# Kernel tuning notes

Hardware: AMD Instinct MI355X
Metric: run time of the kernel (lower is better)

## Reference

```python
import jax, jax.numpy as jnp
import numpy as np

B, K, NV, H, T = 4, 2, 32, 16, 4096
G = K * NV                 # conv groups = 64
OPG = 2 * (NV + H)         # out channels per group = 96 (instantaneous doubles channels)
TEMPERATURE = 1.0


def setup_inputs() -> dict:
    key = jax.random.key(0)
    k1, k2, k3 = jax.random.split(key, 3)
    x = jax.random.normal(k1, (B, G * H, T), dtype=jnp.float32)
    W = jax.random.normal(k2, (G, OPG, H), dtype=jnp.float32) * (1.0 / np.sqrt(H))
    b = jax.random.normal(k3, (G, OPG), dtype=jnp.float32) * 0.01
    return {"x": x, "W": W, "b": b}


def reference(x, W, b):
    # pad one zero step at end of sequence (ConstantPad1d((0,1),0))
    xp = jnp.pad(x, ((0, 0), (0, 0), (0, 1)))            # (B, G*H, T+1)
    xg = xp.reshape(B, G, H, T + 1)
    # TCN modeled as grouped pointwise conv: per-group linear over channel dim
    y = jnp.einsum('bgdt,god->bgot', xg, W) + b[None, :, :, None]  # (B, G, OPG, T+1)
    # split temporal / instantaneous branches with the causal shift
    y = y.reshape(B * K, NV, 2, NV + H, T + 1)
    xt = y[:, :, 0, :, :-1]                               # (B*K, NV, NV+H, T)
    xi = y[:, :, 1, :, 1:]                                # (B*K, NV, NV+H, T)
    # split attention logits (first NV channels) and context (last H channels)
    ctx = jnp.concatenate([xt[:, :, NV:, :], xi[:, :, NV:, :]], axis=1)   # (B*K, 2*NV, H, T)
    att = jnp.concatenate([xt[:, :, :NV, :], xi[:, :, :NV, :]], axis=2)   # (B*K, NV, 2*NV, T)
    att = jax.nn.softmax(att / TEMPERATURE, axis=2)
    out = jnp.einsum('bijt,bjdt->bidt', att, ctx)         # (B*K, NV, H, T)
    out = out.reshape(B, K * NV * H, T)
    attn = att.reshape(B, K, NV, 2 * NV, T)
    return out, attn
```

## Files before the change

kernel.cpp:

```cpp
#include <hip/hip_runtime.h>
#include <stdint.h>

#define T_    4096
#define XGS   74
#define AIS32 33
#define ATS32 1056
#define CTS16 1056
#define RSW   33

typedef _Float16 h2 __attribute__((ext_vector_type(2)));

static __device__ __forceinline__ float dot2(uint32_t a, uint32_t b, float c) {
#if __has_builtin(__builtin_amdgcn_fdot2)
    return __builtin_amdgcn_fdot2(__builtin_bit_cast(h2, a), __builtin_bit_cast(h2, b), c, false);
#else
    h2 ha = __builtin_bit_cast(h2, a), hb = __builtin_bit_cast(h2, b);
    return fmaf((float)ha.x, (float)hb.x, fmaf((float)ha.y, (float)hb.y, c));
#endif
}
static __device__ __forceinline__ float exp2a(float x) {
#if __has_builtin(__builtin_amdgcn_exp2f)
    return __builtin_amdgcn_exp2f(x);
#else
    return exp2f(x);
#endif
}
static __device__ __forceinline__ uint16_t f2h(float f) {
    _Float16 h = (_Float16)f; return __builtin_bit_cast(uint16_t, h);
}
static __device__ __forceinline__ float h2f(uint16_t u) {
    return (float)__builtin_bit_cast(_Float16, u);
}
static __device__ __forceinline__ uint32_t pk2(float lo, float hi) {
    return __builtin_bit_cast(uint32_t, __builtin_amdgcn_cvt_pkrtz(lo, hi));
}
static __device__ __forceinline__ int stg_ix(int rp, int t) {
    return rp * 9 + 2 * (rp >> 4) + t;
}

__global__ __launch_bounds__(512, 2)
void tamcad_kernel(const float* __restrict__ x, const float* __restrict__ W,
                   const float* __restrict__ bias, float* __restrict__ out)
{
    __shared__ uint32_t As32[8448];
    __shared__ uint32_t Cs32[4224];
    __shared__ uint32_t xs32[2368];
    __shared__ uint32_t stg [2336];
    __shared__ float    rs  [264];
    uint16_t* Cs16 = (uint16_t*)Cs32;

    const int tid   = threadIdx.x;
    const int bk    = blockIdx.x >> 6;
    const int chunk = blockIdx.x & 63;
    const int b     = bk >> 1;
    const int k     = bk & 1;

    const int oq   = tid & 15;
    const int g    = tid >> 4;
    const int slot = oq >> 3;

    uint32_t wp2[6][8]; float breg[6]; bool isl[6];
    int cofs[6]; int aofs[3]; bool acat[3];
    #pragma unroll
    for (int r = 0; r < 6; ++r) {
        const int o = oq * 6 + r;
        const float4* wp = reinterpret_cast<const float4*>(W + (((size_t)(k*32+g))*96 + o)*16);
        float4 w0 = wp[0], w1 = wp[1], w2 = wp[2], w3 = wp[3];
        wp2[r][0] = pk2(w0.x, w0.y); wp2[r][1] = pk2(w0.z, w0.w);
        wp2[r][2] = pk2(w1.x, w1.y); wp2[r][3] = pk2(w1.z, w1.w);
        wp2[r][4] = pk2(w2.x, w2.y); wp2[r][5] = pk2(w2.z, w2.w);
        wp2[r][6] = pk2(w3.x, w3.y); wp2[r][7] = pk2(w3.z, w3.w);
        breg[r] = bias[(k*32+g)*96 + o];
        cofs[r] = 0;
        if (o < 32)       isl[r] = true;
        else if (o < 48) { isl[r] = false; cofs[r] = (o-32)*66 + g; }
        else if (o < 80)  isl[r] = true;
        else             { isl[r] = false; cofs[r] = (o-80)*66 + 32 + g; }
    }
    #pragma unroll
    for (int p = 0; p < 3; ++p) {
        const int oe = oq*6 + 2*p;
        if (oe < 32)                   { acat[p] = true;  aofs[p] = g*AIS32 + (oe >> 1); }
        else if (oe >= 48 && oe < 80)  { acat[p] = true;  aofs[p] = g*AIS32 + ((oe-16) >> 1); }
        else                           { acat[p] = false; aofs[p] = 0; }
    }

    const float* xrow = x + ((size_t)b*1024 + (size_t)(k*32+g)*16 + oq) * (size_t)T_;

    float4 pA, pB; float pS;
    {
        const float* gp = xrow + chunk*64;
        pA = *(const float4*)gp; pB = *(const float4*)(gp + 4); pS = gp[8];
    }

    for (int l = 0; l <= 8; ++l) {
        const int t0p = chunk*64 + (l-1)*8;

        if (l > 0) {
            if (tid >= 256) {
                const int q = tid - 256, j = q & 63, jb = j >> 1, jh = j & 1;
                float* attn_base = out + (size_t)4*1024*(size_t)T_;
                #pragma unroll
                for (int rr = 0; rr < 8; ++rr) {
                    const int i = (q >> 6) + 4*rr;
                    float av[8];
                    #pragma unroll
                    for (int u = 0; u < 8; ++u) {
                        uint32_t w = As32[u*ATS32 + i*AIS32 + jb];
                        av[u] = h2f(jh ? (uint16_t)(w >> 16) : (uint16_t)(w & 0xFFFF))
                              * rs[u*RSW + i];
                    }
                    float* tp2 = attn_base + (((size_t)bk*32 + i)*64 + j)*(size_t)T_ + t0p;
                    *(float4*)(tp2+0) = make_float4(av[0],av[1],av[2],av[3]);
                    *(float4*)(tp2+4) = make_float4(av[4],av[5],av[6],av[7]);
                }
            } else {
                const int t  = tid >> 5;
                const int r5 = tid & 31;
                const int i0 = (r5 >> 2) * 4;
                const int d0 = (r5 & 3) * 4;
                const int ab = t*ATS32 + i0*AIS32;
                const int cb = t*528 + d0*33;
                float acc[4][4];
                #pragma unroll
                for (int ii = 0; ii < 4; ++ii)
                    #pragma unroll
                    for (int dd = 0; dd < 4; ++dd) acc[ii][dd] = 0.f;
                #pragma unroll 4
                for (int jp = 0; jp < 32; ++jp) {
                    uint32_t a0 = As32[ab+jp],    a1 = As32[ab+33+jp];
                    uint32_t a2 = As32[ab+66+jp], a3 = As32[ab+99+jp];
                    uint32_t c0 = Cs32[cb+jp],    c1 = Cs32[cb+33+jp];
                    uint32_t c2 = Cs32[cb+66+jp], c3 = Cs32[cb+99+jp];
                    acc[0][0]=dot2(a0,c0,acc[0][0]); acc[0][1]=dot2(a0,c1,acc[0][1]);
                    acc[0][2]=dot2(a0,c2,acc[0][2]); acc[0][3]=dot2(a0,c3,acc[0][3]);
                    acc[1][0]=dot2(a1,c0,acc[1][0]); acc[1][1]=dot2(a1,c1,acc[1][1]);
                    acc[1][2]=dot2(a1,c2,acc[1][2]); acc[1][3]=dot2(a1,c3,acc[1][3]);
                    acc[2][0]=dot2(a2,c0,acc[2][0]); acc[2][1]=dot2(a2,c1,acc[2][1]);
                    acc[2][2]=dot2(a2,c2,acc[2][2]); acc[2][3]=dot2(a2,c3,acc[2][3]);
                    acc[3][0]=dot2(a3,c0,acc[3][0]); acc[3][1]=dot2(a3,c1,acc[3][1]);
                    acc[3][2]=dot2(a3,c2,acc[3][2]); acc[3][3]=dot2(a3,c3,acc[3][3]);
                }
                #pragma unroll
                for (int ii = 0; ii < 4; ++ii) {
                    const float rv = rs[t*RSW + i0 + ii];
                    const int rp = (i0+ii)*8 + (d0 >> 1);
                    stg[stg_ix(rp,   t)] = pk2(acc[ii][0]*rv, acc[ii][1]*rv);
                    stg[stg_ix(rp+1, t)] = pk2(acc[ii][2]*rv, acc[ii][3]*rv);
                }
            }
        }
        if (l < 8) {
            float vals[9] = { pA.x,pA.y,pA.z,pA.w, pB.x,pB.y,pB.z,pB.w, pS };
            #pragma unroll
            for (int i = 0; i < 9; ++i) {
                float mine  = vals[i];
                float other = __shfl_xor(mine, 1);
                if (((i ^ oq) & 1) == 0) {
                    uint32_t pk = (oq & 1) ? pk2(other, mine) : pk2(mine, other);
                    xs32[g*XGS + i*8 + (oq >> 1)] = pk;
                }
            }
            if (l < 7) {
                const int t0n = chunk*64 + (l+1)*8;
                const float* gp = xrow + t0n;
                pA = *(const float4*)gp; pB = *(const float4*)(gp + 4);
                pS = ((t0n + 8) < T_) ? gp[8] : 0.0f;
            }
        }
        __syncthreads();

        if (l > 0) {
            const int rp = tid >> 1, hi = tid & 1, base = stg_ix(rp, 0);
            float ov[8];
            #pragma unroll
            for (int u = 0; u < 8; ++u) {
                uint32_t w = stg[base + u];
                ov[u] = h2f(hi ? (uint16_t)(w >> 16) : (uint16_t)(w & 0xFFFF));
            }
            float* op = out + ((size_t)b*1024 + k*512 + tid)*(size_t)T_ + t0p;
            *(float4*)(op+0) = make_float4(ov[0],ov[1],ov[2],ov[3]);
            *(float4*)(op+4) = make_float4(ov[4],ov[5],ov[6],ov[7]);
        }
        if (l < 8) {
            float asum[8];
            #pragma unroll
            for (int q = 0; q < 8; ++q) {
                const uint32_t* xp = xs32 + g*XGS + (q + slot)*8;
                uint4 xa = *(const uint4*)xp;
                uint4 xb = *(const uint4*)(xp + 4);
                uint32_t xw[8] = { xa.x,xa.y,xa.z,xa.w, xb.x,xb.y,xb.z,xb.w };
                float v[6]; float s = 0.f;
                #pragma unroll
                for (int r = 0; r < 6; ++r) {
                    float y = breg[r];
                    #pragma unroll
                    for (int dd = 0; dd < 8; ++dd) y = dot2(wp2[r][dd], xw[dd], y);
                    const float e = exp2a(fmaf(y, 1.44269504089f, -4.0f));
                    v[r] = isl[r] ? e : y;
                    s   += isl[r] ? e : 0.f;
                }
                #pragma unroll
                for (int p = 0; p < 3; ++p) {
                    if (acat[p]) {
                        As32[q*ATS32 + aofs[p]] = pk2(v[2*p], v[2*p+1]);
                    } else {
                        Cs16[q*CTS16 + cofs[2*p]]   = f2h(v[2*p]);
                        Cs16[q*CTS16 + cofs[2*p+1]] = f2h(v[2*p+1]);
                    }
                }
                asum[q] = s;
            }
            #pragma unroll
            for (int sft = 1; sft < 16; sft <<= 1) {
                #pragma unroll
                for (int q = 0; q < 8; ++q) asum[q] += __shfl_xor(asum[q], sft);
            }
            if (oq == 0) {
                #pragma unroll
                for (int q = 0; q < 8; ++q)
                    rs[q*RSW + g] = __builtin_amdgcn_rcpf(asum[q]);
            }
        }
        if (l < 8) __syncthreads();
    }
}

extern "C" void kernel_launch(void* const* d_in, const int* in_sizes, int n_in,
                              void* d_out, int out_size, void* d_ws, size_t ws_size,
                              hipStream_t stream) {
    const float* x  = (const float*)d_in[0];
    const float* W  = (const float*)d_in[1];
    const float* bs = (const float*)d_in[2];
    float* out = (float*)d_out;
    tamcad_kernel<<<dim3(512), dim3(512), 0, stream>>>(x, W, bs, out);
}
```

Baseline: 285.6 us.

## Double block size to 1024 threads and split per-thread work in half

Moves the block from 512 to 1024 threads. Each thread now computes 3 output channels instead of 6, loads half an x row segment, and handles a 2x4 instead of a 4x4 attention-context tile. The A and C shared buffers are merged into one fp16 array, so every channel does a single scalar fp16 store. The aim is more waves per block to hide latency and fewer registers per thread. The cost is more shuffle-reduction steps, less register reuse per thread, and tighter occupancy limits at 1024 threads.

```diff
diff --git a/kernel.cpp b/kernel.cpp
--- a/kernel.cpp
+++ b/kernel.cpp
@@ -3,9 +3,10 @@
 
 #define T_    4096
 #define XGS   74
-#define AIS32 33
-#define ATS32 1056
+#define ATS16 2112
+#define AIS16 66
 #define CTS16 1056
+#define CSB16 16896
 #define RSW   33
 
 typedef _Float16 h2 __attribute__((ext_vector_type(2)));
@@ -38,16 +39,16 @@
     return rp * 9 + 2 * (rp >> 4) + t;
 }
 
-__global__ __launch_bounds__(512, 2)
+__global__ __launch_bounds__(1024, 4)
 void tamcad_kernel(const float* __restrict__ x, const float* __restrict__ W,
                    const float* __restrict__ bias, float* __restrict__ out)
 {
-    __shared__ uint32_t As32[8448];
-    __shared__ uint32_t Cs32[4224];
+    __shared__ uint16_t ACs16[CSB16 + 8 * CTS16];
     __shared__ uint32_t xs32[2368];
     __shared__ uint32_t stg [2336];
     __shared__ float    rs  [264];
-    uint16_t* Cs16 = (uint16_t*)Cs32;
+    const uint32_t* As32r = (const uint32_t*)ACs16;
+    const uint32_t* Cs32r = (const uint32_t*)(ACs16 + CSB16);
 
     const int tid   = threadIdx.x;
     const int bk    = blockIdx.x >> 6;
@@ -55,15 +56,17 @@
     const int b     = bk >> 1;
     const int k     = bk & 1;
 
-    const int oq   = tid & 15;
-    const int g    = tid >> 4;
-    const int slot = oq >> 3;
-
-    uint32_t wp2[6][8]; float breg[6]; bool isl[6];
-    int cofs[6]; int aofs[3]; bool acat[3];
+    const int g  = tid >> 5;
+    const int m  = tid & 31;
+    const int d  = m >> 1;
+    const int h  = m & 1;
+    const int oq = m;
+    const int slot = m >> 4;
+
+    uint32_t wp2[3][8]; float breg[3]; int sofs[3]; bool isl[3];
     #pragma unroll
-    for (int r = 0; r < 6; ++r) {
-        const int o = oq * 6 + r;
+    for (int r = 0; r < 3; ++r) {
+        const int o = oq * 3 + r;
         const float4* wp = reinterpret_cast<const float4*>(W + (((size_t)(k*32+g))*96 + o)*16);
         float4 w0 = wp[0], w1 = wp[1], w2 = wp[2], w3 = wp[3];
         wp2[r][0] = pk2(w0.x, w0.y); wp2[r][1] = pk2(w0.z, w0.w);
@@ -71,42 +74,64 @@
         wp2[r][4] = pk2(w2.x, w2.y); wp2[r][5] = pk2(w2.z, w2.w);
         wp2[r][6] = pk2(w3.x, w3.y); wp2[r][7] = pk2(w3.z, w3.w);
         breg[r] = bias[(k*32+g)*96 + o];
-        cofs[r] = 0;
-        if (o < 32)       isl[r] = true;
-        else if (o < 48) { isl[r] = false; cofs[r] = (o-32)*66 + g; }
-        else if (o < 80)  isl[r] = true;
-        else             { isl[r] = false; cofs[r] = (o-80)*66 + 32 + g; }
+        if (o < 32)      { isl[r] = true;  sofs[r] = g*AIS16 + o; }
+        else if (o < 48) { isl[r] = false; sofs[r] = CSB16 + (o-32)*AIS16 + g; }
+        else if (o < 80) { isl[r] = true;  sofs[r] = g*AIS16 + (o-16); }
+        else             { isl[r] = false; sofs[r] = CSB16 + (o-80)*AIS16 + 32 + g; }
     }
-    #pragma unroll
-    for (int p = 0; p < 3; ++p) {
-        const int oe = oq*6 + 2*p;
-        if (oe < 32)                   { acat[p] = true;  aofs[p] = g*AIS32 + (oe >> 1); }
-        else if (oe >= 48 && oe < 80)  { acat[p] = true;  aofs[p] = g*AIS32 + ((oe-16) >> 1); }
-        else                           { acat[p] = false; aofs[p] = 0; }
-    }
-
-    const float* xrow = x + ((size_t)b*1024 + (size_t)(k*32+g)*16 + oq) * (size_t)T_;
-
-    float4 pA, pB; float pS;
+
+    const float* xrow = x + ((size_t)b*1024 + (size_t)(k*32+g)*16 + d) * (size_t)T_;
+
+    float4 pA; float pS;
     {
-        const float* gp = xrow + chunk*64;
-        pA = *(const float4*)gp; pB = *(const float4*)(gp + 4); pS = gp[8];
+        const float* gp = xrow + chunk*64 + h*4;
+        pA = *(const float4*)gp;
+        pS = h ? gp[4] : 0.0f;
     }
 
     for (int l = 0; l <= 8; ++l) {
         const int t0p = chunk*64 + (l-1)*8;
 
         if (l > 0) {
-            if (tid >= 256) {
-                const int q = tid - 256, j = q & 63, jb = j >> 1, jh = j & 1;
+            if (tid < 512) {
+                const int t  = tid >> 6;
+                const int r6 = tid & 63;
+                const int i0 = (r6 & 15) * 2;
+                const int d0 = (r6 >> 4) * 4;
+                const int ab = t*1056 + i0*33;
+                const int cb = t*528  + d0*33;
+                float acc[2][4];
+                #pragma unroll
+                for (int ii = 0; ii < 2; ++ii)
+                    #pragma unroll
+                    for (int dd = 0; dd < 4; ++dd) acc[ii][dd] = 0.f;
+                #pragma unroll 4
+                for (int jp = 0; jp < 32; ++jp) {
+                    uint32_t a0 = As32r[ab+jp],    a1 = As32r[ab+33+jp];
+                    uint32_t c0 = Cs32r[cb+jp],    c1 = Cs32r[cb+33+jp];
+                    uint32_t c2 = Cs32r[cb+66+jp], c3 = Cs32r[cb+99+jp];
+                    acc[0][0]=dot2(a0,c0,acc[0][0]); acc[0][1]=dot2(a0,c1,acc[0][1]);
+                    acc[0][2]=dot2(a0,c2,acc[0][2]); acc[0][3]=dot2(a0,c3,acc[0][3]);
+                    acc[1][0]=dot2(a1,c0,acc[1][0]); acc[1][1]=dot2(a1,c1,acc[1][1]);
+                    acc[1][2]=dot2(a1,c2,acc[1][2]); acc[1][3]=dot2(a1,c3,acc[1][3]);
+                }
+                const float rv0 = rs[t*RSW + i0], rv1 = rs[t*RSW + i0 + 1];
+                const int rp0 = i0*8 + (d0 >> 1);
+                stg[stg_ix(rp0,     t)] = pk2(acc[0][0]*rv0, acc[0][1]*rv0);
+                stg[stg_ix(rp0 + 1, t)] = pk2(acc[0][2]*rv0, acc[0][3]*rv0);
+                stg[stg_ix(rp0 + 8, t)] = pk2(acc[1][0]*rv1, acc[1][1]*rv1);
+                stg[stg_ix(rp0 + 9, t)] = pk2(acc[1][2]*rv1, acc[1][3]*rv1);
+            } else {
+                const int q = tid - 512, j = q & 63, jb = j >> 1, jh = j & 1;
+                const int ib = q >> 6;
                 float* attn_base = out + (size_t)4*1024*(size_t)T_;
                 #pragma unroll
-                for (int rr = 0; rr < 8; ++rr) {
-                    const int i = (q >> 6) + 4*rr;
+                for (int rr = 0; rr < 4; ++rr) {
+                    const int i = ib + 8*rr;
                     float av[8];
                     #pragma unroll
                     for (int u = 0; u < 8; ++u) {
-                        uint32_t w = As32[u*ATS32 + i*AIS32 + jb];
+                        uint32_t w = As32r[u*1056 + i*33 + jb];
                         av[u] = h2f(jh ? (uint16_t)(w >> 16) : (uint16_t)(w & 0xFFFF))
                               * rs[u*RSW + i];
                     }
@@ -114,73 +139,43 @@
                     *(float4*)(tp2+0) = make_float4(av[0],av[1],av[2],av[3]);
                     *(float4*)(tp2+4) = make_float4(av[4],av[5],av[6],av[7]);
                 }
-            } else {
-                const int t  = tid >> 5;
-                const int r5 = tid & 31;
-                const int i0 = (r5 >> 2) * 4;
-                const int d0 = (r5 & 3) * 4;
-                const int ab = t*ATS32 + i0*AIS32;
-                const int cb = t*528 + d0*33;
-                float acc[4][4];
-                #pragma unroll
-                for (int ii = 0; ii < 4; ++ii)
-                    #pragma unroll
-                    for (int dd = 0; dd < 4; ++dd) acc[ii][dd] = 0.f;
-                #pragma unroll 4
-                for (int jp = 0; jp < 32; ++jp) {
-                    uint32_t a0 = As32[ab+jp],    a1 = As32[ab+33+jp];
-                    uint32_t a2 = As32[ab+66+jp], a3 = As32[ab+99+jp];
-                    uint32_t c0 = Cs32[cb+jp],    c1 = Cs32[cb+33+jp];
-                    uint32_t c2 = Cs32[cb+66+jp], c3 = Cs32[cb+99+jp];
-                    acc[0][0]=dot2(a0,c0,acc[0][0]); acc[0][1]=dot2(a0,c1,acc[0][1]);
-                    acc[0][2]=dot2(a0,c2,acc[0][2]); acc[0][3]=dot2(a0,c3,acc[0][3]);
-                    acc[1][0]=dot2(a1,c0,acc[1][0]); acc[1][1]=dot2(a1,c1,acc[1][1]);
-                    acc[1][2]=dot2(a1,c2,acc[1][2]); acc[1][3]=dot2(a1,c3,acc[1][3]);
-                    acc[2][0]=dot2(a2,c0,acc[2][0]); acc[2][1]=dot2(a2,c1,acc[2][1]);
-                    acc[2][2]=dot2(a2,c2,acc[2][2]); acc[2][3]=dot2(a2,c3,acc[2][3]);
-                    acc[3][0]=dot2(a3,c0,acc[3][0]); acc[3][1]=dot2(a3,c1,acc[3][1]);
-                    acc[3][2]=dot2(a3,c2,acc[3][2]); acc[3][3]=dot2(a3,c3,acc[3][3]);
-                }
-                #pragma unroll
-                for (int ii = 0; ii < 4; ++ii) {
-                    const float rv = rs[t*RSW + i0 + ii];
-                    const int rp = (i0+ii)*8 + (d0 >> 1);
-                    stg[stg_ix(rp,   t)] = pk2(acc[ii][0]*rv, acc[ii][1]*rv);
-                    stg[stg_ix(rp+1, t)] = pk2(acc[ii][2]*rv, acc[ii][3]*rv);
-                }
             }
         }
         if (l < 8) {
-            float vals[9] = { pA.x,pA.y,pA.z,pA.w, pB.x,pB.y,pB.z,pB.w, pS };
-            #pragma unroll
-            for (int i = 0; i < 9; ++i) {
-                float mine  = vals[i];
-                float other = __shfl_xor(mine, 1);
-                if (((i ^ oq) & 1) == 0) {
-                    uint32_t pk = (oq & 1) ? pk2(other, mine) : pk2(mine, other);
-                    xs32[g*XGS + i*8 + (oq >> 1)] = pk;
+            float va[5] = { pA.x, pA.y, pA.z, pA.w, pS };
+            #pragma unroll
+            for (int i = 0; i < 5; ++i) {
+                if (i == 4 && h == 0) continue;
+                const int u = h*4 + i;
+                const float mine  = va[i];
+                const float other = __shfl_xor(mine, 2);
+                if (((u ^ d) & 1) == 0) {
+                    const uint32_t pk = (d & 1) ? pk2(other, mine) : pk2(mine, other);
+                    xs32[g*XGS + u*8 + (d >> 1)] = pk;
                 }
             }
             if (l < 7) {
                 const int t0n = chunk*64 + (l+1)*8;
-                const float* gp = xrow + t0n;
-                pA = *(const float4*)gp; pB = *(const float4*)(gp + 4);
-                pS = ((t0n + 8) < T_) ? gp[8] : 0.0f;
+                const float* gp = xrow + t0n + h*4;
+                pA = *(const float4*)gp;
+                pS = (h && (t0n + 8) < T_) ? gp[4] : 0.0f;
             }
         }
         __syncthreads();
 
         if (l > 0) {
-            const int rp = tid >> 1, hi = tid & 1, base = stg_ix(rp, 0);
-            float ov[8];
-            #pragma unroll
-            for (int u = 0; u < 8; ++u) {
+            const int r   = tid >> 1;
+            const int th4 = (tid & 1) * 4;
+            const int rp  = r >> 1, hi = r & 1;
+            const int base = stg_ix(rp, th4);
+            float ov[4];
+            #pragma unroll
+            for (int u = 0; u < 4; ++u) {
                 uint32_t w = stg[base + u];
                 ov[u] = h2f(hi ? (uint16_t)(w >> 16) : (uint16_t)(w & 0xFFFF));
             }
-            float* op = out + ((size_t)b*1024 + k*512 + tid)*(size_t)T_ + t0p;
-            *(float4*)(op+0) = make_float4(ov[0],ov[1],ov[2],ov[3]);
-            *(float4*)(op+4) = make_float4(ov[4],ov[5],ov[6],ov[7]);
+            float* op = out + ((size_t)b*1024 + k*512 + r)*(size_t)T_ + t0p + th4;
+            *(float4*)op = make_float4(ov[0], ov[1], ov[2], ov[3]);
         }
         if (l < 8) {
             float asum[8];
@@ -190,29 +185,20 @@
                 uint4 xa = *(const uint4*)xp;
                 uint4 xb = *(const uint4*)(xp + 4);
                 uint32_t xw[8] = { xa.x,xa.y,xa.z,xa.w, xb.x,xb.y,xb.z,xb.w };
-                float v[6]; float s = 0.f;
-                #pragma unroll
-                for (int r = 0; r < 6; ++r) {
+                float s = 0.f;
+                #pragma unroll
+                for (int r = 0; r < 3; ++r) {
                     float y = breg[r];
                     #pragma unroll
                     for (int dd = 0; dd < 8; ++dd) y = dot2(wp2[r][dd], xw[dd], y);
                     const float e = exp2a(fmaf(y, 1.44269504089f, -4.0f));
-                    v[r] = isl[r] ? e : y;
-                    s   += isl[r] ? e : 0.f;
-                }
-                #pragma unroll
-                for (int p = 0; p < 3; ++p) {
-                    if (acat[p]) {
-                        As32[q*ATS32 + aofs[p]] = pk2(v[2*p], v[2*p+1]);
-                    } else {
-                        Cs16[q*CTS16 + cofs[2*p]]   = f2h(v[2*p]);
-                        Cs16[q*CTS16 + cofs[2*p+1]] = f2h(v[2*p+1]);
-                    }
+                    s += isl[r] ? e : 0.f;
+                    ACs16[sofs[r] + q*(isl[r] ? ATS16 : CTS16)] = f2h(isl[r] ? e : y);
                 }
                 asum[q] = s;
             }
             #pragma unroll
-            for (int sft = 1; sft < 16; sft <<= 1) {
+            for (int sft = 1; sft < 32; sft <<= 1) {
                 #pragma unroll
                 for (int q = 0; q < 8; ++q) asum[q] += __shfl_xor(asum[q], sft);
             }
@@ -233,5 +219,5 @@
     const float* W  = (const float*)d_in[1];
     const float* bs = (const float*)d_in[2];
     float* out = (float*)d_out;
-    tamcad_kernel<<<dim3(512), dim3(512), 0, stream>>>(x, W, bs, out);
-}
+    tamcad_kernel<<<dim3(512), dim3(1024), 0, stream>>>(x, W, bs, out);
+}
```

Result: slower. 293.3 us (+2.7%).
